# Kernel optimization log

Measured on AMD Instinct MI355X. Metric: run time of the kernel, lower is better.

The kernel has to match this reference:

```python
import jax, jax.numpy as jnp
import numpy as np
import math

B, S, D, H = 8, 4096, 1024, 16
DH = D // H  # 64

def setup_inputs() -> dict:
    key = jax.random.key(0)
    ks = jax.random.split(key, 5)
    scale = 1.0 / math.sqrt(D)
    return {
        "x": jax.random.normal(ks[0], (B, S, D), dtype=jnp.float32),
        "Wq": jax.random.normal(ks[1], (D, D), dtype=jnp.float32) * scale,
        "Wk": jax.random.normal(ks[2], (D, D), dtype=jnp.float32) * scale,
        "Wv": jax.random.normal(ks[3], (D, D), dtype=jnp.float32) * scale,
        "Wo": jax.random.normal(ks[4], (D, D), dtype=jnp.float32) * scale,
    }

def reference(x, Wq, Wk, Wv, Wo):
    # Linear layers: y = x @ W.T (torch nn.Linear convention, bias=False)
    q = x @ Wq.T  # [B,S,D]
    k = x @ Wk.T
    v = x @ Wv.T
    # split heads -> [B,H,S,DH]
    def split(t):
        return t.reshape(B, S, H, DH).transpose(0, 2, 1, 3)
    q, k, v = split(q), split(k), split(v)
    # QUIRK: scores over head-feature dims: q^T @ k -> [B,H,DH,DH]
    scores = jnp.einsum('bhsd,bhse->bhde', q, k) / math.sqrt(DH)
    att = jax.nn.softmax(scores, axis=-1)  # [B,H,DH,DH]
    # v @ att -> [B,H,S,DH]
    out = jnp.einsum('bhsd,bhde->bhse', v, att)
    out = out.transpose(0, 2, 1, 3).reshape(B, S, D)
    return out @ Wo.T  # [B,S,D]; squeeze(dim=1) is a no-op since S>1
```

## Files before the change

kernel.cpp:

```cpp
#include <hip/hip_runtime.h>
#include <hip/hip_bf16.h>


#define B_ 8
#define S_ 4096
#define D_ 1024
#define H_ 16

typedef unsigned short u16;
typedef __attribute__((ext_vector_type(4))) short short4v;
typedef __attribute__((ext_vector_type(8))) _Float16 half8v;
typedef __attribute__((ext_vector_type(4))) float f32x4;

typedef __attribute__((address_space(3))) unsigned lds_u32_t;
typedef const __attribute__((address_space(1))) unsigned glb_u32_t;

__device__ __forceinline__ unsigned short f2h(float f) {
    _Float16 h = (_Float16)f;
    return __builtin_bit_cast(unsigned short, h);
}
__device__ __forceinline__ float h2f(unsigned short s) {
    return (float)__builtin_bit_cast(_Float16, s);
}
__device__ __forceinline__ void gll16(const u16* g, u16* lds) {
    __builtin_amdgcn_global_load_lds((glb_u32_t*)g, (lds_u32_t*)lds, 16, 0, 0);
}
__device__ __forceinline__ void pair_decode(int pair, int& ti, int& tj) {
    ti = (int)((sqrtf(8.f * pair + 1.f) - 1.f) * 0.5f);
    if ((ti + 1) * (ti + 2) / 2 <= pair) ++ti;
    if (ti * (ti + 1) / 2 > pair) --ti;
    tj = pair - ti * (ti + 1) / 2;
}

__global__ __launch_bounds__(256) void gram_splitk(
    const u16* __restrict__ xt, u16* __restrict__ P)
{
    __shared__ u16 As[128 * 32];
    __shared__ u16 Bs[128 * 32];

    const int l = ((blockIdx.x & 7) * 144) + (blockIdx.x >> 3);
    const int batch = l / 144;
    const int rem = l - batch * 144;
    const int chunk = rem / 36;
    const int pair = rem - chunk * 36;
    int ti, tj;
    pair_decode(pair, ti, tj);

    const int t = threadIdx.x, lane = t & 63, wave = t >> 6;
    const int wm = (wave >> 1) * 64, wn = (wave & 1) * 64;
    const int fr = lane & 15, kg = lane >> 4;

    const u16* Ag = xt + ((long)batch * D_ + ti * 128) * S_ + chunk * 1024;
    const u16* Bg = xt + ((long)batch * D_ + tj * 128) * S_ + chunk * 1024;

    f32x4 acc[4][4];
#pragma unroll
    for (int i = 0; i < 4; ++i)
#pragma unroll
        for (int j = 0; j < 4; ++j) acc[i][j] = (f32x4){0.f, 0.f, 0.f, 0.f};

    for (int k0 = 0; k0 < 1024; k0 += 32) {
        if (k0) __syncthreads();
#pragma unroll
        for (int r = 0; r < 2; ++r) {
            const int off = r * 2048 + t * 8;
            const int row = off >> 5, kc = off & 31;
            gll16(Ag + (long)row * S_ + k0 + kc, As + off);
            gll16(Bg + (long)row * S_ + k0 + kc, Bs + off);
        }
        __syncthreads();

        const int ao = (wm + fr) * 32 + kg * 8;
        const int bo = (wn + fr) * 32 + kg * 8;
        half8v a[4], b[4];
#pragma unroll
        for (int mt = 0; mt < 4; ++mt) a[mt] = *(const half8v*)&As[ao + mt * 512];
#pragma unroll
        for (int nt = 0; nt < 4; ++nt) b[nt] = *(const half8v*)&Bs[bo + nt * 512];
#pragma unroll
        for (int mt = 0; mt < 4; ++mt)
#pragma unroll
            for (int nt = 0; nt < 4; ++nt)
                acc[mt][nt] = __builtin_amdgcn_mfma_f32_16x16x32_f16(a[mt], b[nt], acc[mt][nt], 0, 0, 0);
    }

    u16* out = P + (((long)chunk * B_ + batch) * 36 + pair) * 16384;
#pragma unroll
    for (int mt = 0; mt < 4; ++mt)
#pragma unroll
        for (int nt = 0; nt < 4; ++nt)
#pragma unroll
            for (int q = 0; q < 4; ++q)
                out[(wm + mt * 16 + kg * 4 + q) * 128 + wn + nt * 16 + fr] = f2h(acc[mt][nt][q]);
}

__global__ __launch_bounds__(256) void reduce_mirror(
    const u16* __restrict__ P, u16* __restrict__ G)
{
    __shared__ u16 th[128][132];
    const int pair = blockIdx.x, b = blockIdx.y;
    int ti, tj;
    pair_decode(pair, ti, tj);
    const int t = threadIdx.x;
    const long tile = 16384;
    const long cs = (long)B_ * 36 * tile;
    const u16* base = P + ((long)b * 36 + pair) * tile;
    u16* GB = G + (long)b * D_ * D_;

#pragma unroll
    for (int e = 0; e < 16; ++e) {
        const int idx = e * 1024 + t * 4;
        short4v s0 = *(const short4v*)&base[idx];
        short4v s1 = *(const short4v*)&base[cs + idx];
        short4v s2 = *(const short4v*)&base[2 * cs + idx];
        short4v s3 = *(const short4v*)&base[3 * cs + idx];
        const int r = idx >> 7, c = idx & 127;
        short4v hv;
#pragma unroll
        for (int j = 0; j < 4; ++j) {
            const float f = h2f((u16)s0[j]) + h2f((u16)s1[j]) + h2f((u16)s2[j]) + h2f((u16)s3[j]);
            hv[j] = (short)f2h(f);
        }
        *(short4v*)&GB[(long)(ti * 128 + r) * D_ + tj * 128 + c] = hv;
        if (ti != tj) {
#pragma unroll
            for (int j = 0; j < 4; ++j) th[c + j][r] = (u16)hv[j];
        }
    }
    if (ti != tj) {
        __syncthreads();
#pragma unroll
        for (int e = 0; e < 16; ++e) {
            const int idx = e * 1024 + t * 4;
            const int r = idx >> 7, c = idx & 127;
            short4v hv = *(const short4v*)&th[r][c];
            *(short4v*)&GB[(long)(tj * 128 + r) * D_ + ti * 128 + c] = hv;
        }
    }
}

template<int OUT>
__global__ __launch_bounds__(512) void gemm256x128(
    const u16* __restrict__ A, const u16* __restrict__ B,
    float* __restrict__ Cf, u16* __restrict__ Ch,
    int K, int lda, int ldb, int ldc, long sA, long sB, long sC)
{
    constexpr int BSZ = 12288;
    constexpr int AOF = 0, BOF = 8192;
    __shared__ u16 lds[3 * BSZ];

    const int p = blockIdx.x;
    const int l = (p & 7) * 32 + (p >> 3);
    const int bz = l >> 5;
    const int bm0 = ((l >> 3) & 3) * 256;
    const int bn0 = (l & 7) * 128;

    const int t = threadIdx.x, lane = t & 63, wave = t >> 6;
    const int wm = (wave >> 1) * 64, wn = (wave & 1) * 64;
    const int fr = lane & 15, kg = lane >> 4;
    const int xs = (fr >> 1) & 3;

    const u16* gA = A + (long)bz * sA + (long)bm0 * lda;
    const u16* gB = B + (long)bz * sB + (long)bn0 * ldb;

    f32x4 acc[4][4];
#pragma unroll
    for (int i = 0; i < 4; ++i)
#pragma unroll
        for (int j = 0; j < 4; ++j) acc[i][j] = (f32x4){0.f, 0.f, 0.f, 0.f};

    const int NT = K >> 5;

    auto stage = [&](int tt, int bs) {
        u16* base = &lds[bs * BSZ];
#pragma unroll
        for (int r = 0; r < 2; ++r) {
            const int idx = t + r * 512;
            const int row = idx >> 2, kq = idx & 3;
            const int ks = (kq ^ ((row >> 1) & 3)) << 3;
            gll16(gA + (long)row * lda + tt * 32 + ks, base + AOF + idx * 8);
        }
        {
            const int row = t >> 2, kq = t & 3;
            const int ks = (kq ^ ((row >> 1) & 3)) << 3;
            gll16(gB + (long)row * ldb + tt * 32 + ks, base + BOF + t * 8);
        }
    };

    stage(0, 0);
    stage(1, 1);
    asm volatile("s_waitcnt vmcnt(3)" ::: "memory");
    __builtin_amdgcn_s_barrier();

    for (int tt = 0; tt < NT; ++tt) {
        const u16* base = &lds[(tt % 3) * BSZ];
        if (tt + 2 < NT) stage(tt + 2, (tt + 2) % 3);

        const int ko = (kg ^ xs) << 3;
        half8v a[4], b[4];
#pragma unroll
        for (int mt = 0; mt < 4; ++mt) a[mt] = *(const half8v*)&base[AOF + (wm + mt * 16 + fr) * 32 + ko];
#pragma unroll
        for (int nt = 0; nt < 4; ++nt) b[nt] = *(const half8v*)&base[BOF + (wn + nt * 16 + fr) * 32 + ko];
#pragma unroll
        for (int mt = 0; mt < 4; ++mt)
#pragma unroll
            for (int nt = 0; nt < 4; ++nt)
                acc[mt][nt] = __builtin_amdgcn_mfma_f32_16x16x32_f16(a[mt], b[nt], acc[mt][nt], 0, 0, 0);

        if (tt + 1 < NT) {
            if (tt + 2 < NT) asm volatile("s_waitcnt vmcnt(3)" ::: "memory");
            else             asm volatile("s_waitcnt vmcnt(0)" ::: "memory");
            __builtin_amdgcn_s_barrier();
        }
    }

#pragma unroll
    for (int mt = 0; mt < 4; ++mt)
#pragma unroll
        for (int nt = 0; nt < 4; ++nt)
#pragma unroll
            for (int q = 0; q < 4; ++q) {
                const int row = bm0 + wm + mt * 16 + kg * 4 + q;
                const int col = bn0 + wn + nt * 16 + fr;
                const float v = acc[mt][nt][q];
                const long idx = (long)bz * sC + (long)row * ldc + col;
                if (OUT == 0) Cf[idx] = v;
                else Ch[idx] = f2h(v);
            }
}

__global__ __launch_bounds__(256) void scores_softmax_mfma(
    const u16* __restrict__ M, const u16* __restrict__ Wkh, float* __restrict__ att)
{
    constexpr int BSZ = 4096;
    constexpr int AOF = 0, BOF = 2048;
    __shared__ u16 lds[3 * BSZ];
    __shared__ float Sm[64][68];
    __shared__ float rowm[64], rowsv[64];

    const int bh = blockIdx.x;
    const int b = bh >> 4, h = bh & 15;
    const u16* gA = M + (long)b * D_ * D_ + (long)h * 64 * D_;
    const u16* gB = Wkh + (long)h * 64 * D_;

    const int t = threadIdx.x, lane = t & 63, wave = t >> 6;
    const int fr = lane & 15, kg = lane >> 4;
    const int xs = (fr >> 1) & 3;
    const int wrow = wave * 16;

    f32x4 acc[4];
#pragma unroll
    for (int i = 0; i < 4; ++i) acc[i] = (f32x4){0.f, 0.f, 0.f, 0.f};

    auto stage = [&](int tt, int bs) {
        u16* base = &lds[bs * BSZ];
        const int row = t >> 2, kq = t & 3;
        const int ks = (kq ^ ((row >> 1) & 3)) << 3;
        gll16(gA + (long)row * D_ + tt * 32 + ks, base + AOF + t * 8);
        gll16(gB + (long)row * D_ + tt * 32 + ks, base + BOF + t * 8);
    };

    stage(0, 0);
    stage(1, 1);
    asm volatile("s_waitcnt vmcnt(2)" ::: "memory");
    __builtin_amdgcn_s_barrier();

    const int NT = 32;
    for (int tt = 0; tt < NT; ++tt) {
        const u16* base = &lds[(tt % 3) * BSZ];
        if (tt + 2 < NT) stage(tt + 2, (tt + 2) % 3);

        const int ko = (kg ^ xs) << 3;
        half8v a = *(const half8v*)&base[AOF + (wrow + fr) * 32 + ko];
#pragma unroll
        for (int nt = 0; nt < 4; ++nt) {
            half8v bv = *(const half8v*)&base[BOF + (nt * 16 + fr) * 32 + ko];
            acc[nt] = __builtin_amdgcn_mfma_f32_16x16x32_f16(a, bv, acc[nt], 0, 0, 0);
        }

        if (tt + 1 < NT) {
            if (tt + 2 < NT) asm volatile("s_waitcnt vmcnt(2)" ::: "memory");
            else             asm volatile("s_waitcnt vmcnt(0)" ::: "memory");
            __builtin_amdgcn_s_barrier();
        }
    }

#pragma unroll
    for (int nt = 0; nt < 4; ++nt)
#pragma unroll
        for (int q = 0; q < 4; ++q)
            Sm[wrow + kg * 4 + q][nt * 16 + fr] = acc[nt][q] * 0.125f;
    __syncthreads();

    if (t < 64) {
        float m = -1e30f;
        for (int ee = 0; ee < 64; ++ee) m = fmaxf(m, Sm[t][ee]);
        float s = 0.f;
        for (int ee = 0; ee < 64; ++ee) s += expf(Sm[t][ee] - m);
        rowm[t] = m;
        rowsv[t] = 1.0f / s;
    }
    __syncthreads();
    float* abase = att + (long)bh * 4096;
#pragma unroll
    for (int dd = 0; dd < 16; ++dd) {
        const int d = (t >> 6) * 16 + dd;
        const int e = t & 63;
        abase[d * 64 + e] = expf(Sm[d][e] - rowm[d]) * rowsv[d];
    }
}

__global__ __launch_bounds__(512) void gemm256_f16(
    const u16* __restrict__ A, const u16* __restrict__ B, float* __restrict__ C,
    int K, int lda, int ldb, int ldc, long sA, long sB, long sC)
{
    __shared__ u16 lds[2][2][256 * 64];

    const int p = blockIdx.x;
    const int l = (p & 7) * 64 + (p >> 3);
    const int bz = l >> 6;
    const int bm0 = ((l >> 2) & 15) * 256;
    const int bn0 = (l & 3) * 256;

    const int t = threadIdx.x, lane = t & 63, wave = t >> 6;
    const int wm = (wave >> 2) * 128, wn = (wave & 3) * 64;
    const int fr = lane & 15, kg = lane >> 4;

    const u16* Ag = A + (long)bz * sA + (long)bm0 * lda;
    const u16* Bg = B + (long)bz * sB + (long)bn0 * ldb;

    f32x4 acc[8][4];
#pragma unroll
    for (int i = 0; i < 8; ++i)
#pragma unroll
        for (int j = 0; j < 4; ++j) acc[i][j] = (f32x4){0.f, 0.f, 0.f, 0.f};

    const int NT = K >> 6;

    auto stage = [&](int tt, int s) {
#pragma unroll
        for (int c = 0; c < 4; ++c) {
            const int idx = t + c * 512;
            const int row = idx >> 3;
            const int kq = idx & 7;
            const int ks = (kq ^ ((row >> 1) & 7)) << 3;
            gll16(Ag + (long)row * lda + tt * 64 + ks, &lds[s][0][idx * 8]);
            gll16(Bg + (long)row * ldb + tt * 64 + ks, &lds[s][1][idx * 8]);
        }
    };

    stage(0, 0);
    asm volatile("s_waitcnt vmcnt(0)" ::: "memory");
    __builtin_amdgcn_s_barrier();

    for (int tt = 0; tt < NT; ++tt) {
        const int cur = tt & 1;
        if (tt + 1 < NT) stage(tt + 1, cur ^ 1);

        const u16* As = &lds[cur][0][0];
        const u16* Bs = &lds[cur][1][0];

        __builtin_amdgcn_s_setprio(1);
#pragma unroll
        for (int ks2 = 0; ks2 < 2; ++ks2) {
            half8v bf[4];
#pragma unroll
            for (int nt = 0; nt < 4; ++nt) {
                const int row = wn + nt * 16 + fr;
                const int off = row * 64 + (((ks2 * 4 + kg) ^ ((row >> 1) & 7)) << 3);
                bf[nt] = *(const half8v*)&Bs[off];
            }
#pragma unroll
            for (int mt = 0; mt < 8; ++mt) {
                const int row = wm + mt * 16 + fr;
                const int off = row * 64 + (((ks2 * 4 + kg) ^ ((row >> 1) & 7)) << 3);
                half8v af = *(const half8v*)&As[off];
#pragma unroll
                for (int nt = 0; nt < 4; ++nt)
                    acc[mt][nt] = __builtin_amdgcn_mfma_f32_16x16x32_f16(af, bf[nt], acc[mt][nt], 0, 0, 0);
            }
        }
        __builtin_amdgcn_s_setprio(0);

        asm volatile("s_waitcnt vmcnt(0)" ::: "memory");
        __builtin_amdgcn_s_barrier();
    }

#pragma unroll
    for (int mt = 0; mt < 8; ++mt)
#pragma unroll
        for (int nt = 0; nt < 4; ++nt)
#pragma unroll
            for (int q = 0; q < 4; ++q) {
                const int row = bm0 + wm + mt * 16 + kg * 4 + q;
                const int col = bn0 + wn + nt * 16 + fr;
                C[(long)bz * sC + (long)row * ldc + col] = acc[mt][nt][q];
            }
}

__global__ __launch_bounds__(256) void prepack_all(
    const float* __restrict__ x, u16* __restrict__ xt, u16* __restrict__ xh,
    const float* __restrict__ Wq, const float* __restrict__ Wk, const float* __restrict__ Wo,
    u16* __restrict__ Wqh, u16* __restrict__ Wkh, u16* __restrict__ Woh)
{
    const int bid = blockIdx.x;
    const int t = threadIdx.x;
    if (bid >= 8192) {
        const int wb = bid - 8192;
        const float* src;
        u16* dst;
        if (wb < 1024)      { src = Wq; dst = Wqh; }
        else if (wb < 2048) { src = Wk; dst = Wkh; }
        else                { src = Wo; dst = Woh; }
        const long i = ((long)(wb & 1023) * 256 + t) * 4;
        float4 v = *(const float4*)&src[i];
        short4v hv = {(short)f2h(v.x), (short)f2h(v.y), (short)f2h(v.z), (short)f2h(v.w)};
        *(short4v*)&dst[i] = hv;
        return;
    }

    __shared__ float tile[64][65];
    const int d0 = (bid & 15) * 64;
    const int s0 = ((bid >> 4) & 63) * 64;
    const int b = bid >> 10;
    const float* xb = x + (long)b * S_ * D_;
    const int sr = t >> 4, dc = (t & 15) * 4;
#pragma unroll
    for (int r = 0; r < 4; ++r) {
        const int s = sr + r * 16;
        float4 v = *(const float4*)&xb[(long)(s0 + s) * D_ + d0 + dc];
        tile[dc + 0][s] = v.x;
        tile[dc + 1][s] = v.y;
        tile[dc + 2][s] = v.z;
        tile[dc + 3][s] = v.w;
        short4v hv = {(short)f2h(v.x), (short)f2h(v.y), (short)f2h(v.z), (short)f2h(v.w)};
        *(short4v*)&xh[((long)b * S_ + s0 + s) * D_ + d0 + dc] = hv;
    }
    __syncthreads();
    const int dr = t >> 4, sc = (t & 15) * 4;
    u16* tb = xt + (long)b * D_ * S_;
#pragma unroll
    for (int r = 0; r < 4; ++r) {
        const int d = dr + r * 16;
        short4v hv;
#pragma unroll
        for (int j = 0; j < 4; ++j) hv[j] = (short)f2h(tile[d][sc + j]);
        *(short4v*)&tb[(long)(d0 + d) * S_ + s0 + sc] = hv;
    }
}

__global__ __launch_bounds__(256) void build_T(
    const float* __restrict__ Wv, const float* __restrict__ att, u16* __restrict__ T)
{
    __shared__ float atts[64][65];
    __shared__ float Wvs[64][65];
    const int i0 = blockIdx.x * 64, h = blockIdx.y, b = blockIdx.z;
    const int t = threadIdx.x;
    {
        int row = t >> 2, c4 = (t & 3) * 16;
        const float* ab = att + (((long)b * H_ + h) * 64) * 64;
        const float* wb = Wv + (long)h * 64 * D_ + i0;
#pragma unroll
        for (int r = 0; r < 4; ++r) {
            float4 v = *(const float4*)&ab[row * 64 + c4 + r * 4];
            atts[row][c4 + r * 4 + 0] = v.x;
            atts[row][c4 + r * 4 + 1] = v.y;
            atts[row][c4 + r * 4 + 2] = v.z;
            atts[row][c4 + r * 4 + 3] = v.w;
            float4 w = *(const float4*)&wb[(long)row * D_ + c4 + r * 4];
            Wvs[row][c4 + r * 4 + 0] = w.x;
            Wvs[row][c4 + r * 4 + 1] = w.y;
            Wvs[row][c4 + r * 4 + 2] = w.z;
            Wvs[row][c4 + r * 4 + 3] = w.w;
        }
    }
    __syncthreads();
    const int e = t & 63, ig = t >> 6;
    float acc[16];
#pragma unroll
    for (int i = 0; i < 16; ++i) acc[i] = 0.f;
#pragma unroll 8
    for (int d = 0; d < 64; ++d) {
        float av = atts[d][e];
#pragma unroll
        for (int ii = 0; ii < 16; ++ii)
            acc[ii] = fmaf(Wvs[d][ig * 16 + ii], av, acc[ii]);
    }
    u16* Tb = T + (long)b * D_ * D_;
#pragma unroll
    for (int ii = 0; ii < 16; ++ii) {
        int i = i0 + ig * 16 + ii;
        Tb[(long)i * D_ + h * 64 + e] = f2h(acc[ii]);
    }
}

extern "C" void kernel_launch(void* const* d_in, const int* in_sizes, int n_in,
                              void* d_out, int out_size, void* d_ws, size_t ws_size,
                              hipStream_t stream) {
    const float* x  = (const float*)d_in[0];
    const float* Wq = (const float*)d_in[1];
    const float* Wk = (const float*)d_in[2];
    const float* Wv = (const float*)d_in[3];
    const float* Wo = (const float*)d_in[4];
    float* out = (float*)d_out;

    const long MM = (long)D_ * D_;
    const long XE = (long)B_ * S_ * D_;
    const long GE = (long)B_ * MM;
    const long PB = 4L * B_ * 36 * 16384 * 4;

    u16* xt = (u16*)d_out;

    char* w = (char*)d_ws;
    u16* xh    = (u16*)w;   w += XE * 2;
    u16* P     = (u16*)w;
    u16* Mh    = (u16*)w;   w += PB;
    u16* G     = (u16*)w;   w += GE * 2;
    u16* Eth   = (u16*)w;   w += GE * 2;
    float* att = (float*)w; w += (long)B_ * H_ * 64 * 64 * 4;
    u16* Wqh   = (u16*)w;   w += MM * 2;
    u16* Woh   = (u16*)w;   w += MM * 2;
    u16* Wkh   = (u16*)w;
    u16* Th = G;

    prepack_all<<<8192 + 3072, 256, 0, stream>>>(
        x, xt, xh, Wq, Wk, Wo, Wqh, Wkh, Woh);

    gram_splitk<<<36 * 4 * B_, 256, 0, stream>>>(xt, P);

    reduce_mirror<<<dim3(36, B_), 256, 0, stream>>>(P, G);

    gemm256x128<1><<<256, 512, 0, stream>>>(
        Wqh, G, nullptr, Mh, D_, D_, D_, D_, 0, MM, MM);

    scores_softmax_mfma<<<B_ * H_, 256, 0, stream>>>(Mh, Wkh, att);

    build_T<<<dim3(D_ / 64, H_, B_), 256, 0, stream>>>(Wv, att, Th);

    gemm256x128<1><<<256, 512, 0, stream>>>(
        Woh, Th, nullptr, Eth, D_, D_, D_, D_, 0, MM, MM);

    gemm256_f16<<<(S_ / 256) * (D_ / 256) * B_, 512, 0, stream>>>(
        xh, Eth, out, D_, D_, D_, D_, (long)S_ * D_, MM, (long)S_ * D_);
}
```

Measured before the change: 297.5 us.

## Fuse T construction into scores/softmax kernel using MFMA with pre-transposed Wv

The separate build_T kernel, an FP32 FMA kernel reading the att buffer from global memory, is removed. The scores/softmax kernel now keeps the softmax result in LDS as fp16 and multiplies it by a pre-transposed fp16 Wv using MFMA, writing T directly. Prepack gains extra blocks to transpose and convert Wv. This drops one launch and the att round trip, but the fused stage runs on only 128 blocks and works through 1024 rows serially per block, which may underuse the GPU.

```diff
diff --git a/kernel.cpp b/kernel.cpp
--- a/kernel.cpp
+++ b/kernel.cpp
@@ -230,14 +230,17 @@
             }
 }
 
-__global__ __launch_bounds__(256) void scores_softmax_mfma(
-    const u16* __restrict__ M, const u16* __restrict__ Wkh, float* __restrict__ att)
+__global__ __launch_bounds__(256) void scores_sm_T(
+    const u16* __restrict__ M, const u16* __restrict__ Wkh,
+    const u16* __restrict__ WvT, u16* __restrict__ T)
 {
     constexpr int BSZ = 4096;
     constexpr int AOF = 0, BOF = 2048;
     __shared__ u16 lds[3 * BSZ];
     __shared__ float Sm[64][68];
     __shared__ float rowm[64], rowsv[64];
+    __shared__ u16 attT[64][72];
+    __shared__ u16 Av[2][128 * 64];
 
     const int bh = blockIdx.x;
     const int b = bh >> 4, h = bh & 15;
@@ -302,12 +305,70 @@
         rowsv[t] = 1.0f / s;
     }
     __syncthreads();
-    float* abase = att + (long)bh * 4096;
 #pragma unroll
     for (int dd = 0; dd < 16; ++dd) {
         const int d = (t >> 6) * 16 + dd;
         const int e = t & 63;
-        abase[d * 64 + e] = expf(Sm[d][e] - rowm[d]) * rowsv[d];
+        attT[e][d] = f2h(expf(Sm[d][e] - rowm[d]) * rowsv[d]);
+    }
+    __syncthreads();
+
+    const u16* gAv = WvT + (long)h * 64;
+    u16* Tb = T + (long)b * D_ * D_ + (long)h * 64;
+
+    auto stageA = [&](int it, int s) {
+#pragma unroll
+        for (int r = 0; r < 4; ++r) {
+            const int idx = t + r * 256;
+            const int row = idx >> 3, kq = idx & 7;
+            const int ks = (kq ^ ((row >> 1) & 7)) << 3;
+            gll16(gAv + (long)(it * 128 + row) * D_ + ks, &Av[s][idx * 8]);
+        }
+    };
+
+    stageA(0, 0);
+    asm volatile("s_waitcnt vmcnt(0)" ::: "memory");
+    __builtin_amdgcn_s_barrier();
+
+    for (int it = 0; it < 8; ++it) {
+        const int cur = it & 1;
+        if (it + 1 < 8) stageA(it + 1, cur ^ 1);
+
+        f32x4 accT[2][4];
+#pragma unroll
+        for (int m = 0; m < 2; ++m)
+#pragma unroll
+            for (int nt = 0; nt < 4; ++nt) accT[m][nt] = (f32x4){0.f, 0.f, 0.f, 0.f};
+
+#pragma unroll
+        for (int step = 0; step < 2; ++step) {
+            const int kq = step * 4 + kg;
+            half8v bv[4];
+#pragma unroll
+            for (int nt = 0; nt < 4; ++nt)
+                bv[nt] = *(const half8v*)&attT[nt * 16 + fr][kq * 8];
+#pragma unroll
+            for (int m = 0; m < 2; ++m) {
+                const int rl = wave * 32 + m * 16 + fr;
+                half8v av = *(const half8v*)&Av[cur][rl * 64 + ((kq ^ ((rl >> 1) & 7)) << 3)];
+#pragma unroll
+                for (int nt = 0; nt < 4; ++nt)
+                    accT[m][nt] = __builtin_amdgcn_mfma_f32_16x16x32_f16(av, bv[nt], accT[m][nt], 0, 0, 0);
+            }
+        }
+
+#pragma unroll
+        for (int m = 0; m < 2; ++m)
+#pragma unroll
+            for (int nt = 0; nt < 4; ++nt)
+#pragma unroll
+                for (int q = 0; q < 4; ++q) {
+                    const int ri = it * 128 + wave * 32 + m * 16 + kg * 4 + q;
+                    Tb[(long)ri * D_ + nt * 16 + fr] = f2h(accT[m][nt][q]);
+                }
+
+        asm volatile("s_waitcnt vmcnt(0)" ::: "memory");
+        __builtin_amdgcn_s_barrier();
     }
 }
 
@@ -401,11 +462,41 @@
 
 __global__ __launch_bounds__(256) void prepack_all(
     const float* __restrict__ x, u16* __restrict__ xt, u16* __restrict__ xh,
-    const float* __restrict__ Wq, const float* __restrict__ Wk, const float* __restrict__ Wo,
-    u16* __restrict__ Wqh, u16* __restrict__ Wkh, u16* __restrict__ Woh)
+    const float* __restrict__ Wq, const float* __restrict__ Wk,
+    const float* __restrict__ Wo, const float* __restrict__ Wv,
+    u16* __restrict__ Wqh, u16* __restrict__ Wkh, u16* __restrict__ Woh,
+    u16* __restrict__ WvT)
 {
     const int bid = blockIdx.x;
     const int t = threadIdx.x;
+
+    if (bid >= 11264) {
+        __shared__ float tile[64][65];
+        const int wb = bid - 11264;
+        const int r0 = (wb >> 4) * 64;
+        const int c0 = (wb & 15) * 64;
+        const int sr = t >> 4, dc = (t & 15) * 4;
+#pragma unroll
+        for (int r = 0; r < 4; ++r) {
+            const int s = sr + r * 16;
+            float4 v = *(const float4*)&Wv[(long)(r0 + s) * D_ + c0 + dc];
+            tile[dc + 0][s] = v.x;
+            tile[dc + 1][s] = v.y;
+            tile[dc + 2][s] = v.z;
+            tile[dc + 3][s] = v.w;
+        }
+        __syncthreads();
+        const int dr = t >> 4, sc = (t & 15) * 4;
+#pragma unroll
+        for (int r = 0; r < 4; ++r) {
+            const int d = dr + r * 16;
+            short4v hv;
+#pragma unroll
+            for (int j = 0; j < 4; ++j) hv[j] = (short)f2h(tile[d][sc + j]);
+            *(short4v*)&WvT[(long)(c0 + d) * D_ + r0 + sc] = hv;
+        }
+        return;
+    }
     if (bid >= 8192) {
         const int wb = bid - 8192;
         const float* src;
@@ -450,51 +541,6 @@
     }
 }
 
-__global__ __launch_bounds__(256) void build_T(
-    const float* __restrict__ Wv, const float* __restrict__ att, u16* __restrict__ T)
-{
-    __shared__ float atts[64][65];
-    __shared__ float Wvs[64][65];
-    const int i0 = blockIdx.x * 64, h = blockIdx.y, b = blockIdx.z;
-    const int t = threadIdx.x;
-    {
-        int row = t >> 2, c4 = (t & 3) * 16;
-        const float* ab = att + (((long)b * H_ + h) * 64) * 64;
-        const float* wb = Wv + (long)h * 64 * D_ + i0;
-#pragma unroll
-        for (int r = 0; r < 4; ++r) {
-            float4 v = *(const float4*)&ab[row * 64 + c4 + r * 4];
-            atts[row][c4 + r * 4 + 0] = v.x;
-            atts[row][c4 + r * 4 + 1] = v.y;
-            atts[row][c4 + r * 4 + 2] = v.z;
-            atts[row][c4 + r * 4 + 3] = v.w;
-            float4 w = *(const float4*)&wb[(long)row * D_ + c4 + r * 4];
-            Wvs[row][c4 + r * 4 + 0] = w.x;
-            Wvs[row][c4 + r * 4 + 1] = w.y;
-            Wvs[row][c4 + r * 4 + 2] = w.z;
-            Wvs[row][c4 + r * 4 + 3] = w.w;
-        }
-    }
-    __syncthreads();
-    const int e = t & 63, ig = t >> 6;
-    float acc[16];
-#pragma unroll
-    for (int i = 0; i < 16; ++i) acc[i] = 0.f;
-#pragma unroll 8
-    for (int d = 0; d < 64; ++d) {
-        float av = atts[d][e];
-#pragma unroll
-        for (int ii = 0; ii < 16; ++ii)
-            acc[ii] = fmaf(Wvs[d][ig * 16 + ii], av, acc[ii]);
-    }
-    u16* Tb = T + (long)b * D_ * D_;
-#pragma unroll
-    for (int ii = 0; ii < 16; ++ii) {
-        int i = i0 + ig * 16 + ii;
-        Tb[(long)i * D_ + h * 64 + e] = f2h(acc[ii]);
-    }
-}
-
 extern "C" void kernel_launch(void* const* d_in, const int* in_sizes, int n_in,
                               void* d_out, int out_size, void* d_ws, size_t ws_size,
                               hipStream_t stream) {
@@ -518,14 +564,14 @@
     u16* Mh    = (u16*)w;   w += PB;
     u16* G     = (u16*)w;   w += GE * 2;
     u16* Eth   = (u16*)w;   w += GE * 2;
-    float* att = (float*)w; w += (long)B_ * H_ * 64 * 64 * 4;
+    u16* WvT   = (u16*)w;   w += MM * 2;
     u16* Wqh   = (u16*)w;   w += MM * 2;
     u16* Woh   = (u16*)w;   w += MM * 2;
     u16* Wkh   = (u16*)w;
     u16* Th = G;
 
-    prepack_all<<<8192 + 3072, 256, 0, stream>>>(
-        x, xt, xh, Wq, Wk, Wo, Wqh, Wkh, Woh);
+    prepack_all<<<8192 + 3072 + 256, 256, 0, stream>>>(
+        x, xt, xh, Wq, Wk, Wo, Wv, Wqh, Wkh, Woh, WvT);
 
     gram_splitk<<<36 * 4 * B_, 256, 0, stream>>>(xt, P);
 
@@ -534,9 +580,7 @@
     gemm256x128<1><<<256, 512, 0, stream>>>(
         Wqh, G, nullptr, Mh, D_, D_, D_, D_, 0, MM, MM);
 
-    scores_softmax_mfma<<<B_ * H_, 256, 0, stream>>>(Mh, Wkh, att);
-
-    build_T<<<dim3(D_ / 64, H_, B_), 256, 0, stream>>>(Wv, att, Th);
+    scores_sm_T<<<B_ * H_, 256, 0, stream>>>(Mh, Wkh, WvT, Th);
 
     gemm256x128<1><<<256, 512, 0, stream>>>(
         Woh, Th, nullptr, Eth, D_, D_, D_, D_, 0, MM, MM);
```

New measurement: 275.4 us. 7.4% less time.
